# Kernel optimization log

Measured on AMD Instinct MI355X. Metric: run time of the kernel, lower is better.

The kernel has to match this reference:

```python
import jax, jax.numpy as jnp
import numpy as np

B, S, H = 1, 2048, 1024
NH, NKV, HD = 16, 4, 64
I, E, K = 2816, 8, 2
WIN = 512
EPS = 1e-5


def setup_inputs() -> dict:
    key = jax.random.key(0)
    ks = jax.random.split(key, 8)
    sd = 0.02
    return {
        "hidden_states": jax.random.normal(ks[0], (B, S, H), jnp.float32),
        "positions": jnp.arange(S, dtype=jnp.int64),
        "w_qkv": jax.random.normal(ks[1], ((NH + 2 * NKV) * HD, H), jnp.float32) * sd,
        "w_o": jax.random.normal(ks[2], (H, NH * HD), jnp.float32) * sd,
        "router_w": jax.random.normal(ks[3], (E, H), jnp.float32) * sd,
        "ws": jax.random.normal(ks[4], (E, 2 * I, H), jnp.float32) * sd,
        "w2s": jax.random.normal(ks[5], (E, H, I), jnp.float32) * sd,
        "ln1_w": jnp.ones((H,), jnp.float32),
        "ln2_w": jnp.ones((H,), jnp.float32),
    }


def _rmsnorm(x, w):
    return x * jax.lax.rsqrt(jnp.mean(x * x, axis=-1, keepdims=True) + EPS) * w


def reference(hidden_states, positions, w_qkv, w_o, router_w, ws, w2s, ln1_w, ln2_w):
    # residual is None on entry -> residual = input, then input_layernorm
    residual = hidden_states
    x = _rmsnorm(hidden_states, ln1_w)

    # qkv projection (torch Linear: y = x @ W.T), GQA split
    qkv = jnp.einsum("bsh,oh->bso", x, w_qkv)
    q_size, kv_size = NH * HD, NKV * HD
    q = qkv[..., :q_size].reshape(B, S, NH, HD)
    k = qkv[..., q_size:q_size + kv_size].reshape(B, S, NKV, HD)
    v = qkv[..., q_size + kv_size:].reshape(B, S, NKV, HD)
    rep = NH // NKV
    k = jnp.repeat(k, rep, axis=2)  # [B,S,NH,HD]
    v = jnp.repeat(v, rep, axis=2)

    scale = HD ** -0.5
    scores = jnp.einsum("bqhd,bkhd->bhqk", q, k) * scale
    i = jnp.arange(S)[:, None]
    j = jnp.arange(S)[None, :]
    mask = (j <= i) & ((i - j) < WIN)  # causal sliding window
    scores = jnp.where(mask, scores, jnp.finfo(scores.dtype).min)
    attn = jax.nn.softmax(scores, axis=-1)
    o = jnp.einsum("bhqk,bkhd->bqhd", attn, v).reshape(B, S, NH * HD)
    attn_out = jnp.einsum("bso,ho->bsh", o, w_o)

    # pre_moe_layernorm with residual: x += residual; residual = x; x = norm(x)
    x2 = attn_out + residual
    residual2 = x2
    h = _rmsnorm(x2, ln2_w)

    # MoE: router softmax, top-k (renormalize=False), per-expert SwiGLU FFN
    t = h.reshape(-1, H)  # [T,H]
    logits = jnp.einsum("th,eh->te", t, router_w)
    probs = jax.nn.softmax(logits, axis=-1)
    vals, idx = jax.lax.top_k(probs, K)  # [T,K]
    w_dense = jnp.sum(vals[:, :, None] * jax.nn.one_hot(idx, E, dtype=t.dtype), axis=1)  # [T,E]

    out = jnp.zeros_like(t)
    for e in range(E):
        gu = jnp.einsum("th,ih->ti", t, ws[e])  # [T,2I]
        g, u = gu[:, :I], gu[:, I:]
        a = jax.nn.silu(g) * u
        y = jnp.einsum("ti,hi->th", a, w2s[e])
        out = out + w_dense[:, e:e + 1] * y

    return out.reshape(B, S, H), residual2
```

## Files before the change

kernel.cpp:

```cpp
#include <hip/hip_runtime.h>
#include <stdint.h>

typedef unsigned short u16;
typedef __attribute__((ext_vector_type(8))) short short8;
typedef __attribute__((ext_vector_type(4))) float f32x4;

constexpr int SEQ   = 2048;
constexpr int HID   = 1024;
constexpr int NHEAD = 16;
constexpr int QKVD  = 1536;
constexpr int FFI   = 2816;
constexpr int NEXP  = 8;
constexpr int WINSZ = 512;
#define EPSF 1e-5f

__device__ __forceinline__ float bf2f(u16 u) {
  union { unsigned int i; float f; } v; v.i = ((unsigned int)u) << 16; return v.f;
}
__device__ __forceinline__ u16 f2bf(float f) {
  union { unsigned int i; float f; } v; v.f = f;
  unsigned int i = v.i;
  return (u16)((i + 0x7fffu + ((i >> 16) & 1u)) >> 16);
}

__device__ __forceinline__ void gload_lds16(const void* g, void* l) {
  __builtin_amdgcn_global_load_lds((__attribute__((address_space(1))) void*)g,
                                   (__attribute__((address_space(3))) void*)l,
                                   16, 0, 0);
}

#define MFMA_BF16(a, b, c) __builtin_amdgcn_mfma_f32_16x16x32_bf16(a, b, c, 0, 0, 0)

__global__ __launch_bounds__(256) void k_f2b(const float* __restrict__ src,
                                             u16* __restrict__ dst, int n4) {
  int i = blockIdx.x * 256 + threadIdx.x;
  if (i < n4) {
    float4 v = ((const float4*)src)[i];
    ushort4 o;
    o.x = f2bf(v.x); o.y = f2bf(v.y); o.z = f2bf(v.z); o.w = f2bf(v.w);
    ((ushort4*)dst)[i] = o;
  }
}

__global__ __launch_bounds__(256) void k_rmsnorm(const float* __restrict__ x,
                                                 const float* __restrict__ w,
                                                 u16* __restrict__ y) {
  const int tkn = blockIdx.x, tid = threadIdx.x, wid = tid >> 6, lane = tid & 63;
  const float* xr = x + (size_t)tkn * HID;
  float4 v = *(const float4*)&xr[tid * 4];
  float ss = v.x * v.x + v.y * v.y + v.z * v.z + v.w * v.w;
#pragma unroll
  for (int m = 1; m < 64; m <<= 1) ss += __shfl_xor(ss, m);
  __shared__ float red[4];
  if (lane == 0) red[wid] = ss;
  __syncthreads();
  ss = red[0] + red[1] + red[2] + red[3];
  float sc = rsqrtf(ss * (1.0f / HID) + EPSF);
  float4 wv = *(const float4*)&w[tid * 4];
  ushort4 o;
  o.x = f2bf(v.x * sc * wv.x);
  o.y = f2bf(v.y * sc * wv.y);
  o.z = f2bf(v.z * sc * wv.z);
  o.w = f2bf(v.w * sc * wv.w);
  *(ushort4*)&y[(size_t)tkn * HID + tid * 4] = o;
}

template <int MODE>
__global__ __launch_bounds__(256, 2) void k_gemm_bt(
    const u16* __restrict__ A, const u16* __restrict__ B, u16* __restrict__ C,
    int M, int N, int K, const float* __restrict__ resid, float* __restrict__ x2f) {
  __shared__ u16 As[128 * 64];
  __shared__ u16 Bs[128 * 64];
  const int tid = threadIdx.x, wid = tid >> 6, lane = tid & 63;
  const int quad = lane >> 4, l16 = lane & 15;
  const int wr = wid >> 1, wc = wid & 1;
  const int m0 = blockIdx.y * 128, n0 = blockIdx.x * 128;
  const int sr = lane >> 3, sc = (lane & 7) * 8;
  f32x4 acc[4][4] = {};
  const int KT = K >> 6;
  for (int kt = 0; kt < KT; ++kt) {
    const int k0 = kt << 6;
#pragma unroll
    for (int it = 0; it < 4; ++it) {
      int seg = wid * 4 + it;
      int row = seg * 8 + sr;
      gload_lds16(&A[(size_t)(m0 + row) * K + k0 + sc], &As[seg * 512]);
      gload_lds16(&B[(size_t)(n0 + row) * K + k0 + sc], &Bs[seg * 512]);
    }
    __syncthreads();
#pragma unroll
    for (int ks = 0; ks < 2; ++ks) {
      short8 af[4], bf[4];
#pragma unroll
      for (int t = 0; t < 4; ++t)
        af[t] = *(const short8*)&As[(64 * wr + 16 * t + l16) * 64 + ks * 32 + quad * 8];
#pragma unroll
      for (int t = 0; t < 4; ++t)
        bf[t] = *(const short8*)&Bs[(64 * wc + 16 * t + l16) * 64 + ks * 32 + quad * 8];
#pragma unroll
      for (int mt = 0; mt < 4; ++mt)
#pragma unroll
        for (int nt = 0; nt < 4; ++nt)
          acc[mt][nt] = MFMA_BF16(af[mt], bf[nt], acc[mt][nt]);
    }
    __syncthreads();
  }
#pragma unroll
  for (int mt = 0; mt < 4; ++mt)
#pragma unroll
    for (int r = 0; r < 4; ++r) {
      int row = m0 + 64 * wr + 16 * mt + quad * 4 + r;
#pragma unroll
      for (int nt = 0; nt < 4; ++nt) {
        int col = n0 + 64 * wc + 16 * nt + l16;
        float v = acc[mt][nt][r];
        if (MODE == 1) {
          x2f[(size_t)row * N + col] = v + resid[(size_t)row * N + col];
        } else {
          C[(size_t)row * N + col] = f2bf(v);
        }
      }
    }
}

__global__ __launch_bounds__(256, 2) void k_attn(const u16* __restrict__ qkv,
                                                 u16* __restrict__ o) {
  const int qb = blockIdx.x;
  const int h = blockIdx.y;
  const int q0 = qb * 64;
  const int g = h >> 2;
  __shared__ u16 Qs[64 * 72], Ks[64 * 72], Vt[64 * 72], Ps[64 * 72];
  const int tid = threadIdx.x, wid = tid >> 6, lane = tid & 63;
  const int quad = lane >> 4, l16 = lane & 15;

#pragma unroll
  for (int it = 0; it < 2; ++it) {
    int idx = it * 256 + tid;
    int row = idx >> 3, c8 = (idx & 7) * 8;
    *(short8*)&Qs[row * 72 + c8] =
        *(const short8*)&qkv[(size_t)(q0 + row) * QKVD + h * 64 + c8];
  }

  f32x4 oacc[4] = {};
  float mrun[4], lrun[4];
#pragma unroll
  for (int r = 0; r < 4; ++r) { mrun[r] = -1e30f; lrun[r] = 0.f; }

  const int ktlo = (q0 >= WINSZ) ? ((q0 - WINSZ + 1) >> 6) : 0;
  const int kthi = qb;
  for (int kt = ktlo; kt <= kthi; ++kt) {
#pragma unroll
    for (int it = 0; it < 2; ++it) {
      int idx = it * 256 + tid;
      int row = idx >> 3, c8 = (idx & 7) * 8;
      *(short8*)&Ks[row * 72 + c8] =
          *(const short8*)&qkv[(size_t)(kt * 64 + row) * QKVD + 1024 + g * 64 + c8];
    }
#pragma unroll
    for (int it = 0; it < 8; ++it) {
      int idx = it * 256 + tid;
      int key = idx >> 5;
      int d = (idx & 31) * 2;
      unsigned int u = *(const unsigned int*)&qkv[(size_t)(kt * 64 + key) * QKVD + 1280 + g * 64 + d];
      Vt[d * 72 + key] = (u16)(u & 0xffffu);
      Vt[(d + 1) * 72 + key] = (u16)(u >> 16);
    }
    __syncthreads();

    f32x4 sa[4] = {};
#pragma unroll
    for (int ks = 0; ks < 2; ++ks) {
      short8 af = *(const short8*)&Qs[(16 * wid + l16) * 72 + ks * 32 + quad * 8];
#pragma unroll
      for (int ct = 0; ct < 4; ++ct) {
        short8 bf = *(const short8*)&Ks[(16 * ct + l16) * 72 + ks * 32 + quad * 8];
        sa[ct] = MFMA_BF16(af, bf, sa[ct]);
      }
    }

    float pvv[4][4];
#pragma unroll
    for (int r = 0; r < 4; ++r) {
      int i = q0 + 16 * wid + quad * 4 + r;
      float mx = -1e30f;
#pragma unroll
      for (int ct = 0; ct < 4; ++ct) {
        int j = kt * 64 + 16 * ct + l16;
        float v = sa[ct][r] * 0.125f;
        bool ok = (j <= i) && (i - j < WINSZ);
        v = ok ? v : -1e30f;
        pvv[ct][r] = v;
        mx = fmaxf(mx, v);
      }
#pragma unroll
      for (int m = 1; m < 16; m <<= 1) mx = fmaxf(mx, __shfl_xor(mx, m));
      float mnew = fmaxf(mrun[r], mx);
      float alpha = __expf(mrun[r] - mnew);
      float s = 0.f;
#pragma unroll
      for (int ct = 0; ct < 4; ++ct) {
        float p = (pvv[ct][r] > -1e29f) ? __expf(pvv[ct][r] - mnew) : 0.f;
        pvv[ct][r] = p;
        s += p;
      }
#pragma unroll
      for (int m = 1; m < 16; m <<= 1) s += __shfl_xor(s, m);
      lrun[r] = lrun[r] * alpha + s;
      mrun[r] = mnew;
#pragma unroll
      for (int ct = 0; ct < 4; ++ct) oacc[ct][r] *= alpha;
    }
#pragma unroll
    for (int ct = 0; ct < 4; ++ct)
#pragma unroll
      for (int r = 0; r < 4; ++r)
        Ps[(16 * wid + quad * 4 + r) * 72 + 16 * ct + l16] = f2bf(pvv[ct][r]);
    __syncthreads();

#pragma unroll
    for (int ks = 0; ks < 2; ++ks) {
      short8 af = *(const short8*)&Ps[(16 * wid + l16) * 72 + ks * 32 + quad * 8];
#pragma unroll
      for (int ct = 0; ct < 4; ++ct) {
        short8 bf = *(const short8*)&Vt[(16 * ct + l16) * 72 + ks * 32 + quad * 8];
        oacc[ct] = MFMA_BF16(af, bf, oacc[ct]);
      }
    }
    __syncthreads();
  }

#pragma unroll
  for (int ct = 0; ct < 4; ++ct)
#pragma unroll
    for (int r = 0; r < 4; ++r) {
      int row = q0 + 16 * wid + quad * 4 + r;
      float v = oacc[ct][r] / lrun[r];
      o[(size_t)row * HID + h * 64 + 16 * ct + l16] = f2bf(v);
    }
}

__global__ __launch_bounds__(256) void k_rms2_router(
    const float* __restrict__ x2f, const float* __restrict__ ln2,
    const float* __restrict__ rw, u16* __restrict__ T, int* __restrict__ counts,
    int* __restrict__ tok_idx, float* __restrict__ tok_w) {
  const int tkn = blockIdx.x, tid = threadIdx.x, wid = tid >> 6, lane = tid & 63;
  const float* xr = x2f + (size_t)tkn * HID;
  float4 v = *(const float4*)&xr[tid * 4];
  float ss = v.x * v.x + v.y * v.y + v.z * v.z + v.w * v.w;
#pragma unroll
  for (int m = 1; m < 64; m <<= 1) ss += __shfl_xor(ss, m);
  __shared__ float red[4];
  if (lane == 0) red[wid] = ss;
  __syncthreads();
  ss = red[0] + red[1] + red[2] + red[3];
  float sc = rsqrtf(ss * (1.0f / HID) + EPSF);
  float4 lw = *(const float4*)&ln2[tid * 4];
  float t0 = v.x * sc * lw.x;
  float t1 = v.y * sc * lw.y;
  float t2 = v.z * sc * lw.z;
  float t3 = v.w * sc * lw.w;
  ushort4 o;
  o.x = f2bf(t0); o.y = f2bf(t1); o.z = f2bf(t2); o.w = f2bf(t3);
  *(ushort4*)&T[(size_t)tkn * HID + tid * 4] = o;

  float p[8];
#pragma unroll
  for (int e = 0; e < 8; ++e) {
    float4 r = *(const float4*)&rw[e * HID + tid * 4];
    p[e] = t0 * r.x + t1 * r.y + t2 * r.z + t3 * r.w;
  }
#pragma unroll
  for (int e = 0; e < 8; ++e)
#pragma unroll
    for (int m = 1; m < 64; m <<= 1) p[e] += __shfl_xor(p[e], m);
  __shared__ float pr[4][8];
  if (lane == 0)
#pragma unroll
    for (int e = 0; e < 8; ++e) pr[wid][e] = p[e];
  __syncthreads();
  if (tid == 0) {
    float lg[8];
#pragma unroll
    for (int e = 0; e < 8; ++e) lg[e] = pr[0][e] + pr[1][e] + pr[2][e] + pr[3][e];
    float mx = lg[0];
#pragma unroll
    for (int e = 1; e < 8; ++e) mx = fmaxf(mx, lg[e]);
    float ex[8], se = 0.f;
#pragma unroll
    for (int e = 0; e < 8; ++e) { ex[e] = __expf(lg[e] - mx); se += ex[e]; }
    int b0 = 0;
#pragma unroll
    for (int e = 1; e < 8; ++e) if (lg[e] > lg[b0]) b0 = e;
    int b1 = (b0 == 0) ? 1 : 0;
#pragma unroll
    for (int e = 0; e < 8; ++e) if (e != b0 && lg[e] > lg[b1]) b1 = e;
    float inv = 1.0f / se;
    int s0 = atomicAdd(&counts[b0], 1);
    tok_idx[b0 * SEQ + s0] = tkn;
    tok_w[b0 * SEQ + s0] = ex[b0] * inv;
    int s1 = atomicAdd(&counts[b1], 1);
    tok_idx[b1 * SEQ + s1] = tkn;
    tok_w[b1 * SEQ + s1] = ex[b1] * inv;
  }
}

__global__ void k_offsets(const int* __restrict__ counts, int* __restrict__ offs) {
  if (threadIdx.x == 0 && blockIdx.x == 0) {
    int s = 0;
    for (int e = 0; e < NEXP; ++e) { offs[e] = s; s += counts[e]; }
    offs[NEXP] = s;
  }
}

__global__ __launch_bounds__(256, 2) void k_moe_gu(
    const u16* __restrict__ T, const u16* __restrict__ Wgu,
    const int* __restrict__ counts, const int* __restrict__ offs,
    const int* __restrict__ tok_idx, u16* __restrict__ Abuf) {
  const int e = blockIdx.z;
  const int cnt = counts[e];
  const int m0 = blockIdx.y * 128;
  if (m0 >= cnt) return;
  const int n0 = blockIdx.x * 128;
  const u16* We = Wgu + (size_t)e * 2 * FFI * HID;
  const int* ti = tok_idx + e * SEQ;
  const int aoff = offs[e];
  __shared__ u16 As[128 * 64], Bg[128 * 64], Bu[128 * 64];
  const int tid = threadIdx.x, wid = tid >> 6, lane = tid & 63;
  const int quad = lane >> 4, l16 = lane & 15;
  const int wr = wid >> 1, wc = wid & 1;
  const int sr = lane >> 3, sc = (lane & 7) * 8;
  int tokrow[4];
#pragma unroll
  for (int it = 0; it < 4; ++it) {
    int row = (wid * 4 + it) * 8 + sr;
    int ra = m0 + row;
    if (ra > cnt - 1) ra = cnt - 1;
    tokrow[it] = ti[ra];
  }
  f32x4 accg[4][4] = {}, accu[4][4] = {};
  for (int kt = 0; kt < 16; ++kt) {
    const int k0 = kt << 6;
#pragma unroll
    for (int it = 0; it < 4; ++it) {
      int seg = wid * 4 + it;
      int row = seg * 8 + sr;
      gload_lds16(&T[(size_t)tokrow[it] * HID + k0 + sc], &As[seg * 512]);
      gload_lds16(&We[(size_t)(n0 + row) * HID + k0 + sc], &Bg[seg * 512]);
      gload_lds16(&We[(size_t)(FFI + n0 + row) * HID + k0 + sc], &Bu[seg * 512]);
    }
    __syncthreads();
#pragma unroll
    for (int ks = 0; ks < 2; ++ks) {
      short8 af[4], bg[4], bu[4];
#pragma unroll
      for (int t = 0; t < 4; ++t)
        af[t] = *(const short8*)&As[(64 * wr + 16 * t + l16) * 64 + ks * 32 + quad * 8];
#pragma unroll
      for (int t = 0; t < 4; ++t)
        bg[t] = *(const short8*)&Bg[(64 * wc + 16 * t + l16) * 64 + ks * 32 + quad * 8];
#pragma unroll
      for (int t = 0; t < 4; ++t)
        bu[t] = *(const short8*)&Bu[(64 * wc + 16 * t + l16) * 64 + ks * 32 + quad * 8];
#pragma unroll
      for (int mt = 0; mt < 4; ++mt)
#pragma unroll
        for (int nt = 0; nt < 4; ++nt) {
          accg[mt][nt] = MFMA_BF16(af[mt], bg[nt], accg[mt][nt]);
          accu[mt][nt] = MFMA_BF16(af[mt], bu[nt], accu[mt][nt]);
        }
    }
    __syncthreads();
  }
#pragma unroll
  for (int mt = 0; mt < 4; ++mt)
#pragma unroll
    for (int r = 0; r < 4; ++r) {
      int rl = 64 * wr + 16 * mt + quad * 4 + r;
      int grow = m0 + rl;
      if (grow < cnt) {
        size_t rbase = (size_t)(aoff + grow) * FFI;
#pragma unroll
        for (int nt = 0; nt < 4; ++nt) {
          int col = n0 + 64 * wc + 16 * nt + l16;
          float gv = accg[mt][nt][r];
          float uv = accu[mt][nt][r];
          float a = gv / (1.0f + __expf(-gv)) * uv;
          Abuf[rbase + col] = f2bf(a);
        }
      }
    }
}

__global__ __launch_bounds__(256, 2) void k_moe_y(
    const u16* __restrict__ Abuf, const u16* __restrict__ W2,
    const int* __restrict__ counts, const int* __restrict__ offs,
    const int* __restrict__ tok_idx, const float* __restrict__ tok_w,
    float* __restrict__ outf) {
  const int e = blockIdx.z;
  const int cnt = counts[e];
  const int m0 = blockIdx.y * 128;
  if (m0 >= cnt) return;
  const int n0 = blockIdx.x * 128;
  const u16* We = W2 + (size_t)e * HID * FFI;
  const int aoff = offs[e];
  __shared__ u16 As[128 * 64], Bs[128 * 64];
  const int tid = threadIdx.x, wid = tid >> 6, lane = tid & 63;
  const int quad = lane >> 4, l16 = lane & 15;
  const int wr = wid >> 1, wc = wid & 1;
  const int sr = lane >> 3, sc = (lane & 7) * 8;
  int arow[4];
#pragma unroll
  for (int it = 0; it < 4; ++it) {
    int row = (wid * 4 + it) * 8 + sr;
    int ra = m0 + row;
    if (ra > cnt - 1) ra = cnt - 1;
    arow[it] = aoff + ra;
  }
  f32x4 acc[4][4] = {};
  for (int kt = 0; kt < FFI / 64; ++kt) {
    const int k0 = kt << 6;
#pragma unroll
    for (int it = 0; it < 4; ++it) {
      int seg = wid * 4 + it;
      int row = seg * 8 + sr;
      gload_lds16(&Abuf[(size_t)arow[it] * FFI + k0 + sc], &As[seg * 512]);
      gload_lds16(&We[(size_t)(n0 + row) * FFI + k0 + sc], &Bs[seg * 512]);
    }
    __syncthreads();
#pragma unroll
    for (int ks = 0; ks < 2; ++ks) {
      short8 af[4], bf[4];
#pragma unroll
      for (int t = 0; t < 4; ++t)
        af[t] = *(const short8*)&As[(64 * wr + 16 * t + l16) * 64 + ks * 32 + quad * 8];
#pragma unroll
      for (int t = 0; t < 4; ++t)
        bf[t] = *(const short8*)&Bs[(64 * wc + 16 * t + l16) * 64 + ks * 32 + quad * 8];
#pragma unroll
      for (int mt = 0; mt < 4; ++mt)
#pragma unroll
        for (int nt = 0; nt < 4; ++nt)
          acc[mt][nt] = MFMA_BF16(af[mt], bf[nt], acc[mt][nt]);
    }
    __syncthreads();
  }
#pragma unroll
  for (int mt = 0; mt < 4; ++mt)
#pragma unroll
    for (int r = 0; r < 4; ++r) {
      int rl = 64 * wr + 16 * mt + quad * 4 + r;
      int grow = m0 + rl;
      if (grow < cnt) {
        int tok = tok_idx[e * SEQ + grow];
        float wgt = tok_w[e * SEQ + grow];
        size_t obase = (size_t)tok * HID;
#pragma unroll
        for (int nt = 0; nt < 4; ++nt) {
          int col = n0 + 64 * wc + 16 * nt + l16;
          atomicAdd(&outf[obase + col], wgt * acc[mt][nt][r]);
        }
      }
    }
}

extern "C" void kernel_launch(void* const* d_in, const int* in_sizes, int n_in,
                              void* d_out, int out_size, void* d_ws, size_t ws_size,
                              hipStream_t stream) {
  const float* hs   = (const float*)d_in[0];
  const float* wqkv = (const float*)d_in[2];
  const float* wo   = (const float*)d_in[3];
  const float* rwt  = (const float*)d_in[4];
  const float* wsx  = (const float*)d_in[5];
  const float* w2s  = (const float*)d_in[6];
  const float* ln1  = (const float*)d_in[7];
  const float* ln2  = (const float*)d_in[8];
  float* out0 = (float*)d_out;
  float* out1 = out0 + (size_t)SEQ * HID;

  char* p = (char*)d_ws;
  u16* xn      = (u16*)p;   p += (size_t)SEQ * HID * 2;
  u16* qkv     = (u16*)p;   p += (size_t)SEQ * QKVD * 2;
  u16* ob      = (u16*)p;   p += (size_t)SEQ * HID * 2;
  u16* tb      = (u16*)p;   p += (size_t)SEQ * HID * 2;
  int* counts  = (int*)p;   p += 32;
  int* offs    = (int*)p;   p += 64;
  int* tok_idx = (int*)p;   p += (size_t)NEXP * SEQ * 4;
  float* tok_w = (float*)p; p += (size_t)NEXP * SEQ * 4;
  u16* abuf    = (u16*)p;   p += (size_t)2 * SEQ * FFI * 2;
  u16* wqkv_b  = (u16*)p;   p += (size_t)QKVD * HID * 2;
  u16* wo_b    = (u16*)p;   p += (size_t)HID * HID * 2;
  u16* ws_b    = (u16*)p;   p += (size_t)NEXP * 2 * FFI * HID * 2;
  u16* w2s_b   = (u16*)p;   p += (size_t)NEXP * HID * FFI * 2;

  hipMemsetAsync(counts, 0, 32, stream);
  hipMemsetAsync(out0, 0, (size_t)SEQ * HID * 4, stream);

  {
    int n4;
    n4 = QKVD * HID / 4;
    k_f2b<<<(n4 + 255) / 256, 256, 0, stream>>>(wqkv, wqkv_b, n4);
    n4 = HID * HID / 4;
    k_f2b<<<(n4 + 255) / 256, 256, 0, stream>>>(wo, wo_b, n4);
    n4 = NEXP * 2 * FFI * HID / 4;
    k_f2b<<<(n4 + 255) / 256, 256, 0, stream>>>(wsx, ws_b, n4);
    n4 = NEXP * HID * FFI / 4;
    k_f2b<<<(n4 + 255) / 256, 256, 0, stream>>>(w2s, w2s_b, n4);
  }

  k_rmsnorm<<<SEQ, 256, 0, stream>>>(hs, ln1, xn);
  k_gemm_bt<0><<<dim3(QKVD / 128, SEQ / 128), 256, 0, stream>>>(
      xn, wqkv_b, qkv, SEQ, QKVD, HID, nullptr, nullptr);
  k_attn<<<dim3(SEQ / 64, NHEAD), 256, 0, stream>>>(qkv, ob);
  k_gemm_bt<1><<<dim3(HID / 128, SEQ / 128), 256, 0, stream>>>(
      ob, wo_b, nullptr, SEQ, HID, HID, hs, out1);
  k_rms2_router<<<SEQ, 256, 0, stream>>>(out1, ln2, rwt, tb, counts, tok_idx, tok_w);
  k_offsets<<<1, 64, 0, stream>>>(counts, offs);
  k_moe_gu<<<dim3(FFI / 128, SEQ / 128, NEXP), 256, 0, stream>>>(
      tb, ws_b, counts, offs, tok_idx, abuf);
  k_moe_y<<<dim3(HID / 128, SEQ / 128, NEXP), 256, 0, stream>>>(
      abuf, w2s_b, counts, offs, tok_idx, tok_w, out0);
}
```

Baseline: 766.3 us.

## Split-K dense and MoE GEMMs, narrow gate/up tiles, merge weight casts

Merges the four weight fp32-to-bf16 conversion launches into one kernel. The QKV and output-projection GEMMs now use a 2-way split-K that writes fp32 partials. For QKV, a separate pass sums the partials and casts to bf16. For the output projection, the partial sum and residual add move into the RMSNorm/router kernel. The MoE gate/up kernel uses 64-wide N tiles with a higher occupancy hint, and the down-projection uses a 4-way split-K over the intermediate dimension. This adds more blocks to fill the GPU, at the cost of extra fp32 partial traffic, more atomics into the output, and one added launch.

```diff
diff --git a/kernel.cpp b/kernel.cpp
--- a/kernel.cpp
+++ b/kernel.cpp
@@ -31,15 +31,28 @@
 
 #define MFMA_BF16(a, b, c) __builtin_amdgcn_mfma_f32_16x16x32_bf16(a, b, c, 0, 0, 0)
 
-__global__ __launch_bounds__(256) void k_f2b(const float* __restrict__ src,
-                                             u16* __restrict__ dst, int n4) {
+constexpr int CN1 = QKVD * HID / 4;
+constexpr int CN2 = HID * HID / 4;
+constexpr int CN3 = NEXP * 2 * FFI * HID / 4;
+constexpr int CN4 = NEXP * HID * FFI / 4;
+constexpr int CNT_ALL = CN1 + CN2 + CN3 + CN4;
+
+__global__ __launch_bounds__(256) void k_f2b_all(
+    const float* __restrict__ wqkv, const float* __restrict__ wo,
+    const float* __restrict__ ws, const float* __restrict__ w2s,
+    u16* __restrict__ dq, u16* __restrict__ dwo,
+    u16* __restrict__ dws, u16* __restrict__ dw2) {
   int i = blockIdx.x * 256 + threadIdx.x;
-  if (i < n4) {
-    float4 v = ((const float4*)src)[i];
-    ushort4 o;
-    o.x = f2bf(v.x); o.y = f2bf(v.y); o.z = f2bf(v.z); o.w = f2bf(v.w);
-    ((ushort4*)dst)[i] = o;
-  }
+  if (i >= CNT_ALL) return;
+  const float* s; u16* d; int j = i;
+  if (j < CN1) { s = wqkv; d = dq; }
+  else if ((j -= CN1) < CN2) { s = wo; d = dwo; }
+  else if ((j -= CN2) < CN3) { s = ws; d = dws; }
+  else { j -= CN3; s = w2s; d = dw2; }
+  float4 v = ((const float4*)s)[j];
+  ushort4 o;
+  o.x = f2bf(v.x); o.y = f2bf(v.y); o.z = f2bf(v.z); o.w = f2bf(v.w);
+  ((ushort4*)d)[j] = o;
 }
 
 __global__ __launch_bounds__(256) void k_rmsnorm(const float* __restrict__ x,
@@ -65,21 +78,22 @@
   *(ushort4*)&y[(size_t)tkn * HID + tid * 4] = o;
 }
 
-template <int MODE>
-__global__ __launch_bounds__(256, 2) void k_gemm_bt(
-    const u16* __restrict__ A, const u16* __restrict__ B, u16* __restrict__ C,
-    int M, int N, int K, const float* __restrict__ resid, float* __restrict__ x2f) {
+__global__ __launch_bounds__(256, 2) void k_gemm_bt_sk(
+    const u16* __restrict__ A, const u16* __restrict__ B, float* __restrict__ Cf,
+    int N, int K, int Kc) {
   __shared__ u16 As[128 * 64];
   __shared__ u16 Bs[128 * 64];
   const int tid = threadIdx.x, wid = tid >> 6, lane = tid & 63;
   const int quad = lane >> 4, l16 = lane & 15;
   const int wr = wid >> 1, wc = wid & 1;
   const int m0 = blockIdx.y * 128, n0 = blockIdx.x * 128;
+  const int M = gridDim.y * 128;
+  const int kbase = blockIdx.z * Kc;
   const int sr = lane >> 3, sc = (lane & 7) * 8;
   f32x4 acc[4][4] = {};
-  const int KT = K >> 6;
+  const int KT = Kc >> 6;
   for (int kt = 0; kt < KT; ++kt) {
-    const int k0 = kt << 6;
+    const int k0 = kbase + (kt << 6);
 #pragma unroll
     for (int it = 0; it < 4; ++it) {
       int seg = wid * 4 + it;
@@ -105,6 +119,7 @@
     }
     __syncthreads();
   }
+  float* Co = Cf + (size_t)blockIdx.z * M * N;
 #pragma unroll
   for (int mt = 0; mt < 4; ++mt)
 #pragma unroll
@@ -113,14 +128,22 @@
 #pragma unroll
       for (int nt = 0; nt < 4; ++nt) {
         int col = n0 + 64 * wc + 16 * nt + l16;
-        float v = acc[mt][nt][r];
-        if (MODE == 1) {
-          x2f[(size_t)row * N + col] = v + resid[(size_t)row * N + col];
-        } else {
-          C[(size_t)row * N + col] = f2bf(v);
-        }
-      }
-    }
+        Co[(size_t)row * N + col] = acc[mt][nt][r];
+      }
+    }
+}
+
+__global__ __launch_bounds__(256) void k_sum2_bf16(const float* __restrict__ a,
+                                                   const float* __restrict__ b,
+                                                   u16* __restrict__ o, int n4) {
+  int i = blockIdx.x * 256 + threadIdx.x;
+  if (i >= n4) return;
+  float4 x = ((const float4*)a)[i];
+  float4 y = ((const float4*)b)[i];
+  ushort4 u;
+  u.x = f2bf(x.x + y.x); u.y = f2bf(x.y + y.y);
+  u.z = f2bf(x.z + y.z); u.w = f2bf(x.w + y.w);
+  ((ushort4*)o)[i] = u;
 }
 
 __global__ __launch_bounds__(256, 2) void k_attn(const u16* __restrict__ qkv,
@@ -240,12 +263,20 @@
 }
 
 __global__ __launch_bounds__(256) void k_rms2_router(
-    const float* __restrict__ x2f, const float* __restrict__ ln2,
-    const float* __restrict__ rw, u16* __restrict__ T, int* __restrict__ counts,
+    const float* __restrict__ o0, const float* __restrict__ o1,
+    const float* __restrict__ hs, const float* __restrict__ ln2,
+    const float* __restrict__ rw, float* __restrict__ out1,
+    u16* __restrict__ T, int* __restrict__ counts,
     int* __restrict__ tok_idx, float* __restrict__ tok_w) {
   const int tkn = blockIdx.x, tid = threadIdx.x, wid = tid >> 6, lane = tid & 63;
-  const float* xr = x2f + (size_t)tkn * HID;
-  float4 v = *(const float4*)&xr[tid * 4];
+  const size_t base = (size_t)tkn * HID + tid * 4;
+  float4 a = *(const float4*)&o0[base];
+  float4 b = *(const float4*)&o1[base];
+  float4 h = *(const float4*)&hs[base];
+  float4 v;
+  v.x = a.x + b.x + h.x; v.y = a.y + b.y + h.y;
+  v.z = a.z + b.z + h.z; v.w = a.w + b.w + h.w;
+  *(float4*)&out1[base] = v;
   float ss = v.x * v.x + v.y * v.y + v.z * v.z + v.w * v.w;
 #pragma unroll
   for (int m = 1; m < 64; m <<= 1) ss += __shfl_xor(ss, m);
@@ -312,7 +343,7 @@
   }
 }
 
-__global__ __launch_bounds__(256, 2) void k_moe_gu(
+__global__ __launch_bounds__(256, 3) void k_moe_gu(
     const u16* __restrict__ T, const u16* __restrict__ Wgu,
     const int* __restrict__ counts, const int* __restrict__ offs,
     const int* __restrict__ tok_idx, u16* __restrict__ Abuf) {
@@ -320,11 +351,11 @@
   const int cnt = counts[e];
   const int m0 = blockIdx.y * 128;
   if (m0 >= cnt) return;
-  const int n0 = blockIdx.x * 128;
+  const int n0 = blockIdx.x * 64;
   const u16* We = Wgu + (size_t)e * 2 * FFI * HID;
   const int* ti = tok_idx + e * SEQ;
   const int aoff = offs[e];
-  __shared__ u16 As[128 * 64], Bg[128 * 64], Bu[128 * 64];
+  __shared__ u16 As[128 * 64], Bg[64 * 64], Bu[64 * 64];
   const int tid = threadIdx.x, wid = tid >> 6, lane = tid & 63;
   const int quad = lane >> 4, l16 = lane & 15;
   const int wr = wid >> 1, wc = wid & 1;
@@ -337,34 +368,37 @@
     if (ra > cnt - 1) ra = cnt - 1;
     tokrow[it] = ti[ra];
   }
-  f32x4 accg[4][4] = {}, accu[4][4] = {};
+  f32x4 accg[4][2] = {}, accu[4][2] = {};
   for (int kt = 0; kt < 16; ++kt) {
     const int k0 = kt << 6;
 #pragma unroll
     for (int it = 0; it < 4; ++it) {
       int seg = wid * 4 + it;
+      gload_lds16(&T[(size_t)tokrow[it] * HID + k0 + sc], &As[seg * 512]);
+    }
+#pragma unroll
+    for (int it = 0; it < 2; ++it) {
+      int seg = wid * 2 + it;
       int row = seg * 8 + sr;
-      gload_lds16(&T[(size_t)tokrow[it] * HID + k0 + sc], &As[seg * 512]);
       gload_lds16(&We[(size_t)(n0 + row) * HID + k0 + sc], &Bg[seg * 512]);
       gload_lds16(&We[(size_t)(FFI + n0 + row) * HID + k0 + sc], &Bu[seg * 512]);
     }
     __syncthreads();
 #pragma unroll
     for (int ks = 0; ks < 2; ++ks) {
-      short8 af[4], bg[4], bu[4];
+      short8 af[4], bg[2], bu[2];
 #pragma unroll
       for (int t = 0; t < 4; ++t)
         af[t] = *(const short8*)&As[(64 * wr + 16 * t + l16) * 64 + ks * 32 + quad * 8];
 #pragma unroll
-      for (int t = 0; t < 4; ++t)
-        bg[t] = *(const short8*)&Bg[(64 * wc + 16 * t + l16) * 64 + ks * 32 + quad * 8];
-#pragma unroll
-      for (int t = 0; t < 4; ++t)
-        bu[t] = *(const short8*)&Bu[(64 * wc + 16 * t + l16) * 64 + ks * 32 + quad * 8];
+      for (int t = 0; t < 2; ++t) {
+        bg[t] = *(const short8*)&Bg[(32 * wc + 16 * t + l16) * 64 + ks * 32 + quad * 8];
+        bu[t] = *(const short8*)&Bu[(32 * wc + 16 * t + l16) * 64 + ks * 32 + quad * 8];
+      }
 #pragma unroll
       for (int mt = 0; mt < 4; ++mt)
 #pragma unroll
-        for (int nt = 0; nt < 4; ++nt) {
+        for (int nt = 0; nt < 2; ++nt) {
           accg[mt][nt] = MFMA_BF16(af[mt], bg[nt], accg[mt][nt]);
           accu[mt][nt] = MFMA_BF16(af[mt], bu[nt], accu[mt][nt]);
         }
@@ -380,8 +414,8 @@
       if (grow < cnt) {
         size_t rbase = (size_t)(aoff + grow) * FFI;
 #pragma unroll
-        for (int nt = 0; nt < 4; ++nt) {
-          int col = n0 + 64 * wc + 16 * nt + l16;
+        for (int nt = 0; nt < 2; ++nt) {
+          int col = n0 + 32 * wc + 16 * nt + l16;
           float gv = accg[mt][nt][r];
           float uv = accu[mt][nt][r];
           float a = gv / (1.0f + __expf(-gv)) * uv;
@@ -396,11 +430,13 @@
     const int* __restrict__ counts, const int* __restrict__ offs,
     const int* __restrict__ tok_idx, const float* __restrict__ tok_w,
     float* __restrict__ outf) {
-  const int e = blockIdx.z;
+  const int e = blockIdx.z >> 2;
+  const int sk = blockIdx.z & 3;
   const int cnt = counts[e];
   const int m0 = blockIdx.y * 128;
   if (m0 >= cnt) return;
   const int n0 = blockIdx.x * 128;
+  const int kbase = sk * 704;
   const u16* We = W2 + (size_t)e * HID * FFI;
   const int aoff = offs[e];
   __shared__ u16 As[128 * 64], Bs[128 * 64];
@@ -417,8 +453,8 @@
     arow[it] = aoff + ra;
   }
   f32x4 acc[4][4] = {};
-  for (int kt = 0; kt < FFI / 64; ++kt) {
-    const int k0 = kt << 6;
+  for (int kt = 0; kt < 11; ++kt) {
+    const int k0 = kbase + (kt << 6);
 #pragma unroll
     for (int it = 0; it < 4; ++it) {
       int seg = wid * 4 + it;
@@ -481,7 +517,7 @@
   u16* xn      = (u16*)p;   p += (size_t)SEQ * HID * 2;
   u16* qkv     = (u16*)p;   p += (size_t)SEQ * QKVD * 2;
   u16* ob      = (u16*)p;   p += (size_t)SEQ * HID * 2;
-  u16* tb      = (u16*)p;   p += (size_t)SEQ * HID * 2;
+  float* qkvf  = (float*)p; p += (size_t)2 * SEQ * QKVD * 4;
   int* counts  = (int*)p;   p += 32;
   int* offs    = (int*)p;   p += 64;
   int* tok_idx = (int*)p;   p += (size_t)NEXP * SEQ * 4;
@@ -492,31 +528,29 @@
   u16* ws_b    = (u16*)p;   p += (size_t)NEXP * 2 * FFI * HID * 2;
   u16* w2s_b   = (u16*)p;   p += (size_t)NEXP * HID * FFI * 2;
 
+  u16* tb      = xn;
+  float* oacc0 = qkvf;
+  float* oacc1 = qkvf + (size_t)SEQ * HID;
+
   hipMemsetAsync(counts, 0, 32, stream);
   hipMemsetAsync(out0, 0, (size_t)SEQ * HID * 4, stream);
 
-  {
-    int n4;
-    n4 = QKVD * HID / 4;
-    k_f2b<<<(n4 + 255) / 256, 256, 0, stream>>>(wqkv, wqkv_b, n4);
-    n4 = HID * HID / 4;
-    k_f2b<<<(n4 + 255) / 256, 256, 0, stream>>>(wo, wo_b, n4);
-    n4 = NEXP * 2 * FFI * HID / 4;
-    k_f2b<<<(n4 + 255) / 256, 256, 0, stream>>>(wsx, ws_b, n4);
-    n4 = NEXP * HID * FFI / 4;
-    k_f2b<<<(n4 + 255) / 256, 256, 0, stream>>>(w2s, w2s_b, n4);
-  }
+  k_f2b_all<<<(CNT_ALL + 255) / 256, 256, 0, stream>>>(
+      wqkv, wo, wsx, w2s, wqkv_b, wo_b, ws_b, w2s_b);
 
   k_rmsnorm<<<SEQ, 256, 0, stream>>>(hs, ln1, xn);
-  k_gemm_bt<0><<<dim3(QKVD / 128, SEQ / 128), 256, 0, stream>>>(
-      xn, wqkv_b, qkv, SEQ, QKVD, HID, nullptr, nullptr);
+  k_gemm_bt_sk<<<dim3(QKVD / 128, SEQ / 128, 2), 256, 0, stream>>>(
+      xn, wqkv_b, qkvf, QKVD, HID, 512);
+  k_sum2_bf16<<<(SEQ * QKVD / 4 + 255) / 256, 256, 0, stream>>>(
+      qkvf, qkvf + (size_t)SEQ * QKVD, qkv, SEQ * QKVD / 4);
   k_attn<<<dim3(SEQ / 64, NHEAD), 256, 0, stream>>>(qkv, ob);
-  k_gemm_bt<1><<<dim3(HID / 128, SEQ / 128), 256, 0, stream>>>(
-      ob, wo_b, nullptr, SEQ, HID, HID, hs, out1);
-  k_rms2_router<<<SEQ, 256, 0, stream>>>(out1, ln2, rwt, tb, counts, tok_idx, tok_w);
+  k_gemm_bt_sk<<<dim3(HID / 128, SEQ / 128, 2), 256, 0, stream>>>(
+      ob, wo_b, oacc0, HID, HID, 512);
+  k_rms2_router<<<SEQ, 256, 0, stream>>>(oacc0, oacc1, hs, ln2, rwt, out1, tb,
+                                         counts, tok_idx, tok_w);
   k_offsets<<<1, 64, 0, stream>>>(counts, offs);
-  k_moe_gu<<<dim3(FFI / 128, SEQ / 128, NEXP), 256, 0, stream>>>(
+  k_moe_gu<<<dim3(FFI / 64, SEQ / 128, NEXP), 256, 0, stream>>>(
       tb, ws_b, counts, offs, tok_idx, abuf);
-  k_moe_y<<<dim3(HID / 128, SEQ / 128, NEXP), 256, 0, stream>>>(
+  k_moe_y<<<dim3(HID / 128, SEQ / 128, NEXP * 4), 256, 0, stream>>>(
       abuf, w2s_b, counts, offs, tok_idx, tok_w, out0);
 }
```

New measurement: 661.3 us. -13.7%, faster.
